# Performance work log

Measured on AMD Instinct MI355X. Metric: run time of the kernel, lower is better.

Reference implementation:

```python
import jax, jax.numpy as jnp
import numpy as np

S, DIM, DE = 8192, 256, 256


def setup_inputs() -> dict:
    key = jax.random.key(0)
    kx, kq, kk, kv = jax.random.split(key, 4)
    x = jax.random.normal(kx, (S, DE), dtype=jnp.float32)
    # tf.random_normal_initializer() default: stddev=0.05
    Wq = jax.random.normal(kq, (DIM, DE), dtype=jnp.float32) * 0.05
    Wk = jax.random.normal(kk, (DIM, DE), dtype=jnp.float32) * 0.05
    Wv = jax.random.normal(kv, (DE, DE), dtype=jnp.float32) * 0.05
    return {"x": x, "Wq": Wq, "Wk": Wk, "Wv": Wv}


def reference(x, Wq, Wk, Wv):
    # x: [S, De]; Wq, Wk: [dim, De]; Wv: [De, De]
    dim = Wq.shape[0]
    Q = Wq @ x.T                                   # [dim, S]
    K = Wk @ x.T                                   # [dim, S]
    score = (Q.T @ K) / jnp.sqrt(jnp.float32(dim))  # [S, S]
    s = score.shape[0]
    # band_part(-1, 0) keeps the lower triangle (causal); zeros elsewhere,
    # then tf.where(score != 0, score, float64.min) -> mask upper triangle
    # with a huge negative (float64.min underflows to -inf in fp32; use fp32 min).
    causal = jnp.tril(jnp.ones((s, s), dtype=bool))
    score = jnp.where(causal, score, jnp.finfo(score.dtype).min)
    attn = jax.nn.softmax(score, axis=1)           # softmax over key axis per row
    V = Wv @ x.T                                   # [De, S]
    deltaE = attn @ V.T                            # [S, De]
    return deltaE
```

## Files before the change

### kernel.cpp

```cpp
#include <hip/hip_runtime.h>
#include <hip/hip_bf16.h>

typedef __attribute__((ext_vector_type(8))) short bf16x8;
typedef __attribute__((ext_vector_type(8))) unsigned short u16x8;
typedef __attribute__((ext_vector_type(4))) float f32x4;

#define SEQ   8192
#define DEM   256
#define CHUNK 512
#define NTASKS 544

#define GLOAD_LDS16(g, l) \
  __builtin_amdgcn_global_load_lds((const __attribute__((address_space(1))) void*)(g), \
                                   (__attribute__((address_space(3))) void*)(l), 16, 0, 0)

static __device__ __forceinline__ unsigned short f2bf(float f) {
  union { float f; unsigned int u; } v; v.f = f;
  return (unsigned short)((v.u + 0x7fffu + ((v.u >> 16) & 1u)) >> 16);
}
static __device__ __forceinline__ float bf2f(unsigned short h) {
  union { unsigned int u; float f; } v; v.u = ((unsigned int)h) << 16;
  return v.f;
}

__global__ __launch_bounds__(256) void proj_kernel(
    const float* __restrict__ x,  const float* __restrict__ Wq,
    const float* __restrict__ Wk, const float* __restrict__ Wv,
    unsigned short* __restrict__ qb, unsigned short* __restrict__ kb,
    unsigned short* __restrict__ vtb)
{
  const int m0 = blockIdx.x * 128;
  const int n0 = blockIdx.y * 128;
  const int which = blockIdx.z;
  const float* __restrict__ W = (which == 0) ? Wq : (which == 1) ? Wk : Wv;

  __shared__ unsigned short As[128 * 64];
  __shared__ unsigned short Bs[128 * 64];

  const int tid  = threadIdx.x;
  const int wave = tid >> 6, lane = tid & 63;
  const int wm = wave >> 1, wn = wave & 1;
  const int lr = lane & 15, lg = lane >> 4;

  f32x4 acc[4][4];
  #pragma unroll
  for (int i = 0; i < 4; i++)
    #pragma unroll
    for (int j = 0; j < 4; j++) acc[i][j] = (f32x4){0.f, 0.f, 0.f, 0.f};

  for (int k0 = 0; k0 < DEM; k0 += 64) {
    __syncthreads();
    #pragma unroll
    for (int p = 0; p < 8; p++) {
      int c   = p * 256 + tid;
      int row = c >> 4;
      int col = (c & 15) << 2;
      float4 fA = *reinterpret_cast<const float4*>(&x[(m0 + row) * DEM + k0 + col]);
      float4 fB = *reinterpret_cast<const float4*>(&W[(n0 + row) * DEM + k0 + col]);
      uint2 hA, hB;
      hA.x = f2bf(fA.x) | ((unsigned)f2bf(fA.y) << 16);
      hA.y = f2bf(fA.z) | ((unsigned)f2bf(fA.w) << 16);
      hB.x = f2bf(fB.x) | ((unsigned)f2bf(fB.y) << 16);
      hB.y = f2bf(fB.z) | ((unsigned)f2bf(fB.w) << 16);
      int byte = (row * 128 + (col << 1)) ^ ((row & 7) << 4);
      *reinterpret_cast<uint2*>(reinterpret_cast<char*>(As) + byte) = hA;
      *reinterpret_cast<uint2*>(reinterpret_cast<char*>(Bs) + byte) = hB;
    }
    __syncthreads();

    #pragma unroll
    for (int ks = 0; ks < 2; ks++) {
      bf16x8 a[4], b[4];
      #pragma unroll
      for (int mt = 0; mt < 4; mt++) {
        int row  = wm * 64 + mt * 16 + lr;
        int byte = (row * 128 + ks * 64 + lg * 16) ^ ((row & 7) << 4);
        a[mt] = *reinterpret_cast<const bf16x8*>(reinterpret_cast<const char*>(As) + byte);
      }
      #pragma unroll
      for (int nt = 0; nt < 4; nt++) {
        int row  = wn * 64 + nt * 16 + lr;
        int byte = (row * 128 + ks * 64 + lg * 16) ^ ((row & 7) << 4);
        b[nt] = *reinterpret_cast<const bf16x8*>(reinterpret_cast<const char*>(Bs) + byte);
      }
      #pragma unroll
      for (int mt = 0; mt < 4; mt++)
        #pragma unroll
        for (int nt = 0; nt < 4; nt++)
          acc[mt][nt] = __builtin_amdgcn_mfma_f32_16x16x32_bf16(a[mt], b[nt], acc[mt][nt], 0, 0, 0);
    }
  }

  const float osc = (which == 0) ? 0.0625f : 1.0f;
  #pragma unroll
  for (int mt = 0; mt < 4; mt++)
    #pragma unroll
    for (int nt = 0; nt < 4; nt++)
      #pragma unroll
      for (int r = 0; r < 4; r++) {
        int row = m0 + wm * 64 + mt * 16 + lg * 4 + r;
        int col = n0 + wn * 64 + nt * 16 + lr;
        unsigned short h = f2bf(acc[mt][nt][r] * osc);
        if (which == 0)      qb[row * DEM + col]  = h;
        else if (which == 1) kb[row * DEM + col]  = h;
        else                 vtb[(size_t)col * SEQ + row] = h;
      }
}

__global__ __launch_bounds__(512, 2) void attn_kernel(
    const unsigned short* __restrict__ qb, const unsigned short* __restrict__ kb,
    const unsigned short* __restrict__ vtb,
    unsigned short* __restrict__ pOb, float* __restrict__ ml)
{
  __shared__ char lds[147456];
  char* Ks = lds;
  char* Vs = lds + 65536;
  char* Ps = lds + 131072;

  const int t = NTASKS - 1 - (int)blockIdx.x;
  int q = 0, s = 0;
  for (;;) { int n = (q >> 2) + 1; if (t < s + n) break; s += n; ++q; }
  const int c = t - s;
  const int kv_lo = c * CHUNK;
  const int kv_hi_blk = min(kv_lo + CHUNK, (q + 1) * 128);

  const int tid = threadIdx.x;
  const int wave = tid >> 6, lane = tid & 63;
  const int lr = lane & 15, lg = lane >> 4;
  const int qrow = q * 128 + wave * 16;
  const int kv_hi_w = min(kv_hi_blk, ((qrow + 16 + 63) >> 6) << 6);
  char* pb = Ps + wave * 2048;

  bf16x8 qf[8];
  {
    const unsigned short* qp = qb + (size_t)(qrow + lr) * DEM + lg * 8;
    #pragma unroll
    for (int ks = 0; ks < 8; ks++) qf[ks] = *reinterpret_cast<const bf16x8*>(qp + ks * 32);
  }

  f32x4 o[16];
  #pragma unroll
  for (int d = 0; d < 16; d++) o[d] = (f32x4){0.f, 0.f, 0.f, 0.f};
  float m_run = -3.0e38f, l_run = 0.f;

  #pragma unroll
  for (int i = 0; i < 4; i++) {
    int sl = i * 8192 + (wave << 10) + (lane << 4);
    int krow = sl >> 9;
    int kin  = (sl & 511) ^ ((krow & 7) << 4);
    GLOAD_LDS16((const char*)kb + (((size_t)(kv_lo + krow)) << 9) + kin,
                Ks + i * 8192 + (wave << 10));
    int vrow = sl >> 7;
    int vin  = (sl & 127) ^ ((vrow & 7) << 4);
    GLOAD_LDS16((const char*)vtb + ((size_t)vrow * SEQ + kv_lo) * 2 + vin,
                Vs + i * 8192 + (wave << 10));
  }
  __syncthreads();

  const int nsteps = (kv_hi_blk - kv_lo) >> 6;
  for (int st = 0; st < nsteps; st++) {
    const int kv0 = kv_lo + (st << 6);
    const int buf = st & 1;
    if (st + 1 < nsteps) {
      #pragma unroll
      for (int i = 0; i < 4; i++) {
        int sl = i * 8192 + (wave << 10) + (lane << 4);
        int krow = sl >> 9;
        int kin  = (sl & 511) ^ ((krow & 7) << 4);
        GLOAD_LDS16((const char*)kb + (((size_t)(kv0 + 64 + krow)) << 9) + kin,
                    Ks + (buf ^ 1) * 32768 + i * 8192 + (wave << 10));
        int vrow = sl >> 7;
        int vin  = (sl & 127) ^ ((vrow & 7) << 4);
        GLOAD_LDS16((const char*)vtb + ((size_t)vrow * SEQ + kv0 + 64) * 2 + vin,
                    Vs + (buf ^ 1) * 32768 + i * 8192 + (wave << 10));
      }
    }

    const bool act = kv0 < kv_hi_w;
    if (act) {
      f32x4 sc[4];
      #pragma unroll
      for (int nt = 0; nt < 4; nt++) sc[nt] = (f32x4){0.f, 0.f, 0.f, 0.f};
      const char* kbase = Ks + buf * 32768;
      __builtin_amdgcn_s_setprio(1);
      #pragma unroll
      for (int ks = 0; ks < 8; ks++)
        #pragma unroll
        for (int nt = 0; nt < 4; nt++) {
          int krow = nt * 16 + lr;
          int byte = krow * 512 + ((ks * 64 + lg * 16) ^ ((krow & 7) << 4));
          bf16x8 kf = *reinterpret_cast<const bf16x8*>(kbase + byte);
          sc[nt] = __builtin_amdgcn_mfma_f32_16x16x32_bf16(kf, qf[ks], sc[nt], 0, 0, 0);
        }
      __builtin_amdgcn_s_setprio(0);

      const int qg = qrow + lr;
      const bool diag = (kv0 + 63 > qrow);
      float sm[16];
      #pragma unroll
      for (int nt = 0; nt < 4; nt++)
        #pragma unroll
        for (int r = 0; r < 4; r++) {
          float v = sc[nt][r];
          if (diag && (kv0 + nt * 16 + lg * 4 + r > qg)) v = -3.0e38f;
          sm[nt * 4 + r] = v;
        }
      float mx = sm[0];
      #pragma unroll
      for (int j = 1; j < 16; j++) mx = fmaxf(mx, sm[j]);
      mx = fmaxf(mx, __shfl_xor(mx, 16));
      mx = fmaxf(mx, __shfl_xor(mx, 32));
      const float mnew = fmaxf(m_run, mx);
      const float cr = __expf(m_run - mnew);
      float e[16], sum = 0.f;
      #pragma unroll
      for (int j = 0; j < 16; j++) { e[j] = __expf(sm[j] - mnew); sum += e[j]; }
      sum += __shfl_xor(sum, 16);
      sum += __shfl_xor(sum, 32);
      m_run = mnew;
      l_run = l_run * cr + sum;

      #pragma unroll
      for (int nt = 0; nt < 4; nt++) {
        uint2 w;
        w.x = (unsigned)f2bf(e[nt * 4 + 0]) | ((unsigned)f2bf(e[nt * 4 + 1]) << 16);
        w.y = (unsigned)f2bf(e[nt * 4 + 2]) | ((unsigned)f2bf(e[nt * 4 + 3]) << 16);
        *reinterpret_cast<uint2*>(pb + (lr * 128 + ((nt * 32 + lg * 8) ^ ((lr & 7) << 4)))) = w;
      }

      float cf[4];
      #pragma unroll
      for (int r = 0; r < 4; r++) cf[r] = __shfl(cr, lg * 4 + r);
      #pragma unroll
      for (int d = 0; d < 16; d++)
        #pragma unroll
        for (int r = 0; r < 4; r++) o[d][r] *= cf[r];

      bf16x8 pf0 = *reinterpret_cast<const bf16x8*>(pb + (lr * 128 + ((lg * 16)      ^ ((lr & 7) << 4))));
      bf16x8 pf1 = *reinterpret_cast<const bf16x8*>(pb + (lr * 128 + ((64 + lg * 16) ^ ((lr & 7) << 4))));
      const char* vbase = Vs + buf * 32768;
      __builtin_amdgcn_s_setprio(1);
      #pragma unroll
      for (int d = 0; d < 16; d++) {
        const int vrow = d * 16 + lr;
        const int vswz = (vrow & 7) << 4;
        bf16x8 v0 = *reinterpret_cast<const bf16x8*>(vbase + vrow * 128 + ((lg * 16)      ^ vswz));
        bf16x8 v1 = *reinterpret_cast<const bf16x8*>(vbase + vrow * 128 + ((64 + lg * 16) ^ vswz));
        o[d] = __builtin_amdgcn_mfma_f32_16x16x32_bf16(pf0, v0, o[d], 0, 0, 0);
        o[d] = __builtin_amdgcn_mfma_f32_16x16x32_bf16(pf1, v1, o[d], 0, 0, 0);
      }
      __builtin_amdgcn_s_setprio(0);
    }
    __syncthreads();
  }

  const size_t obase = (size_t)t * (128 * 256);
  #pragma unroll
  for (int d = 0; d < 16; d++)
    #pragma unroll
    for (int r = 0; r < 4; r++) {
      const int row_l = wave * 16 + lg * 4 + r;
      pOb[obase + (size_t)row_l * 256 + d * 16 + lr] = f2bf(o[d][r]);
    }
  if (lg == 0) {
    const int row_l = wave * 16 + lr;
    ml[(size_t)t * 256 + row_l * 2]     = m_run;
    ml[(size_t)t * 256 + row_l * 2 + 1] = l_run;
  }
}

__global__ __launch_bounds__(256) void merge_kernel(
    const unsigned short* __restrict__ pOb, const float* __restrict__ ml,
    float* __restrict__ out)
{
  const int tid = threadIdx.x;
  const int row = blockIdx.x * 32 + (tid >> 3);
  const int c0  = (tid & 7) * 32;
  const int q = row >> 7;
  const int a = q >> 2, b = q & 3;
  const int n = a + 1;
  const int base = (2 * a + b) * (a + 1);
  const int lrow = row & 127;

  float M = -3.0e38f;
  for (int i = 0; i < n; i++)
    M = fmaxf(M, ml[(size_t)(base + i) * 256 + lrow * 2]);

  float L = 0.f;
  float acc[32];
  #pragma unroll
  for (int j = 0; j < 32; j++) acc[j] = 0.f;

  for (int i = 0; i < n; i++) {
    const float mi = ml[(size_t)(base + i) * 256 + lrow * 2];
    const float li = ml[(size_t)(base + i) * 256 + lrow * 2 + 1];
    const float fi = __expf(mi - M);
    L += li * fi;
    const unsigned short* src = pOb + (size_t)(base + i) * (128 * 256) + (size_t)lrow * 256 + c0;
    #pragma unroll
    for (int v = 0; v < 4; v++) {
      u16x8 u = *reinterpret_cast<const u16x8*>(src + v * 8);
      #pragma unroll
      for (int j = 0; j < 8; j++) acc[v * 8 + j] += bf2f((unsigned short)u[j]) * fi;
    }
  }
  const float inv = 1.f / L;
  #pragma unroll
  for (int v = 0; v < 8; v++) {
    float4 w;
    w.x = acc[v * 4 + 0] * inv; w.y = acc[v * 4 + 1] * inv;
    w.z = acc[v * 4 + 2] * inv; w.w = acc[v * 4 + 3] * inv;
    *reinterpret_cast<float4*>(&out[(size_t)row * 256 + c0 + v * 4]) = w;
  }
}

extern "C" void kernel_launch(void* const* d_in, const int* in_sizes, int n_in,
                              void* d_out, int out_size, void* d_ws, size_t ws_size,
                              hipStream_t stream)
{
  const float* x  = (const float*)d_in[0];
  const float* Wq = (const float*)d_in[1];
  const float* Wk = (const float*)d_in[2];
  const float* Wv = (const float*)d_in[3];

  char* ws = (char*)d_ws;
  unsigned short* qb  = (unsigned short*)ws;
  unsigned short* kb  = (unsigned short*)(ws + (size_t)4  * 1024 * 1024);
  unsigned short* vtb = (unsigned short*)(ws + (size_t)8  * 1024 * 1024);
  float*          ml  = (float*)         (ws + (size_t)12 * 1024 * 1024);
  unsigned short* pOb = (unsigned short*)(ws + (size_t)13 * 1024 * 1024);

  proj_kernel<<<dim3(64, 2, 3), 256, 0, stream>>>(x, Wq, Wk, Wv, qb, kb, vtb);
  attn_kernel<<<dim3(NTASKS), 512, 0, stream>>>(qb, kb, vtb, pOb, ml);
  merge_kernel<<<dim3(SEQ / 32), 256, 0, stream>>>(pOb, ml, (float*)d_out);
}
```

Before: 125.7 us.

## Switch attention to 32x32 MFMA tiles with 256-row query blocks and lazy rescale

Each attention block now covers 256 query rows (32 per wave), which halves the task count. It uses 32x32x16 bf16 MFMA for both the QK^T and PV products, so each K/V tile loaded into LDS is reused across more query rows. The log2(e) factor is folded into the Q scale so the softmax can use exp2 directly. Output rescaling is skipped when the row max grows by no more than a threshold. The merge kernel's indexing is updated to match. The larger per-wave accumulators raise register pressure, and fewer, larger causal tasks may balance less well across CUs.

```diff
diff --git a/kernel.cpp b/kernel.cpp
--- a/kernel.cpp
+++ b/kernel.cpp
@@ -4,11 +4,12 @@
 typedef __attribute__((ext_vector_type(8))) short bf16x8;
 typedef __attribute__((ext_vector_type(8))) unsigned short u16x8;
 typedef __attribute__((ext_vector_type(4))) float f32x4;
+typedef __attribute__((ext_vector_type(16))) float f32x16;
 
 #define SEQ   8192
 #define DEM   256
 #define CHUNK 512
-#define NTASKS 544
+#define NTASKS 272
 
 #define GLOAD_LDS16(g, l) \
   __builtin_amdgcn_global_load_lds((const __attribute__((address_space(1))) void*)(g), \
@@ -91,7 +92,7 @@
     }
   }
 
-  const float osc = (which == 0) ? 0.0625f : 1.0f;
+  const float osc = (which == 0) ? 0.0625f * 1.4426950408889634f : 1.0f;
   #pragma unroll
   for (int mt = 0; mt < 4; mt++)
     #pragma unroll
@@ -119,33 +120,36 @@
 
   const int t = NTASKS - 1 - (int)blockIdx.x;
   int q = 0, s = 0;
-  for (;;) { int n = (q >> 2) + 1; if (t < s + n) break; s += n; ++q; }
+  for (;;) { int n = (q >> 1) + 1; if (t < s + n) break; s += n; ++q; }
   const int c = t - s;
   const int kv_lo = c * CHUNK;
-  const int kv_hi_blk = min(kv_lo + CHUNK, (q + 1) * 128);
+  const int kv_hi_blk = min(kv_lo + CHUNK, (q + 1) * 256);
 
   const int tid = threadIdx.x;
   const int wave = tid >> 6, lane = tid & 63;
-  const int lr = lane & 15, lg = lane >> 4;
-  const int qrow = q * 128 + wave * 16;
-  const int kv_hi_w = min(kv_hi_blk, ((qrow + 16 + 63) >> 6) << 6);
+  const int ql = lane & 31;
+  const int hi = lane >> 5;
+  const int qrow = q * 256 + wave * 32;
+  const int kv_hi_w = min(kv_hi_blk, ((qrow + 32 + 63) >> 6) << 6);
   char* pb = Ps + wave * 2048;
 
-  bf16x8 qf[8];
+  bf16x8 qf[16];
   {
-    const unsigned short* qp = qb + (size_t)(qrow + lr) * DEM + lg * 8;
-    #pragma unroll
-    for (int ks = 0; ks < 8; ks++) qf[ks] = *reinterpret_cast<const bf16x8*>(qp + ks * 32);
-  }
-
-  f32x4 o[16];
-  #pragma unroll
-  for (int d = 0; d < 16; d++) o[d] = (f32x4){0.f, 0.f, 0.f, 0.f};
+    const unsigned short* qp = qb + (size_t)(qrow + ql) * DEM + hi * 8;
+    #pragma unroll
+    for (int i = 0; i < 16; i++) qf[i] = *reinterpret_cast<const bf16x8*>(qp + i * 16);
+  }
+
+  f32x16 o[8];
+  #pragma unroll
+  for (int dt = 0; dt < 8; dt++)
+    #pragma unroll
+    for (int rg = 0; rg < 16; rg++) o[dt][rg] = 0.f;
   float m_run = -3.0e38f, l_run = 0.f;
 
   #pragma unroll
   for (int i = 0; i < 4; i++) {
-    int sl = i * 8192 + (wave << 10) + (lane << 4);
+    int sl = i * 8192 + tid * 16;
     int krow = sl >> 9;
     int kin  = (sl & 511) ^ ((krow & 7) << 4);
     GLOAD_LDS16((const char*)kb + (((size_t)(kv_lo + krow)) << 9) + kin,
@@ -164,7 +168,7 @@
     if (st + 1 < nsteps) {
       #pragma unroll
       for (int i = 0; i < 4; i++) {
-        int sl = i * 8192 + (wave << 10) + (lane << 4);
+        int sl = i * 8192 + tid * 16;
         int krow = sl >> 9;
         int kin  = (sl & 511) ^ ((krow & 7) << 4);
         GLOAD_LDS16((const char*)kb + (((size_t)(kv0 + 64 + krow)) << 9) + kin,
@@ -178,94 +182,114 @@
 
     const bool act = kv0 < kv_hi_w;
     if (act) {
-      f32x4 sc[4];
-      #pragma unroll
-      for (int nt = 0; nt < 4; nt++) sc[nt] = (f32x4){0.f, 0.f, 0.f, 0.f};
+      f32x16 sc0, sc1;
+      #pragma unroll
+      for (int rg = 0; rg < 16; rg++) { sc0[rg] = 0.f; sc1[rg] = 0.f; }
       const char* kbase = Ks + buf * 32768;
+      const int r0 = ql, r1 = 32 + ql;
+      const int rsw = (ql & 7) << 4;
       __builtin_amdgcn_s_setprio(1);
       #pragma unroll
-      for (int ks = 0; ks < 8; ks++)
-        #pragma unroll
-        for (int nt = 0; nt < 4; nt++) {
-          int krow = nt * 16 + lr;
-          int byte = krow * 512 + ((ks * 64 + lg * 16) ^ ((krow & 7) << 4));
-          bf16x8 kf = *reinterpret_cast<const bf16x8*>(kbase + byte);
-          sc[nt] = __builtin_amdgcn_mfma_f32_16x16x32_bf16(kf, qf[ks], sc[nt], 0, 0, 0);
+      for (int i = 0; i < 16; i++) {
+        int off = (i * 32 + hi * 16) ^ rsw;
+        bf16x8 kf0 = *reinterpret_cast<const bf16x8*>(kbase + r0 * 512 + off);
+        bf16x8 kf1 = *reinterpret_cast<const bf16x8*>(kbase + r1 * 512 + off);
+        sc0 = __builtin_amdgcn_mfma_f32_32x32x16_bf16(kf0, qf[i], sc0, 0, 0, 0);
+        sc1 = __builtin_amdgcn_mfma_f32_32x32x16_bf16(kf1, qf[i], sc1, 0, 0, 0);
+      }
+      __builtin_amdgcn_s_setprio(0);
+
+      const int qg = qrow + ql;
+      if (kv0 + 63 > qrow) {
+        #pragma unroll
+        for (int rg = 0; rg < 16; rg++) {
+          int kvp = kv0 + (rg & 3) + 8 * (rg >> 2) + 4 * hi;
+          if (kvp      > qg) sc0[rg] = -3.0e38f;
+          if (kvp + 32 > qg) sc1[rg] = -3.0e38f;
         }
-      __builtin_amdgcn_s_setprio(0);
-
-      const int qg = qrow + lr;
-      const bool diag = (kv0 + 63 > qrow);
-      float sm[16];
-      #pragma unroll
-      for (int nt = 0; nt < 4; nt++)
-        #pragma unroll
-        for (int r = 0; r < 4; r++) {
-          float v = sc[nt][r];
-          if (diag && (kv0 + nt * 16 + lg * 4 + r > qg)) v = -3.0e38f;
-          sm[nt * 4 + r] = v;
+      }
+      float pmax = fmaxf(sc0[0], sc1[0]);
+      #pragma unroll
+      for (int rg = 1; rg < 16; rg++) pmax = fmaxf(pmax, fmaxf(sc0[rg], sc1[rg]));
+      pmax = fmaxf(pmax, __shfl_xor(pmax, 32));
+
+      float mnew;
+      if (__all(pmax <= m_run + 11.0f)) {
+        mnew = m_run;
+      } else {
+        mnew = fmaxf(m_run, pmax);
+        const float cr = __builtin_amdgcn_exp2f(m_run - mnew);
+        #pragma unroll
+        for (int dt = 0; dt < 8; dt++)
+          #pragma unroll
+          for (int rg = 0; rg < 16; rg++) o[dt][rg] *= cr;
+        l_run *= cr;
+        m_run = mnew;
+      }
+
+      float sum = 0.f;
+      uint2 w0[4], w1[4];
+      #pragma unroll
+      for (int tq = 0; tq < 4; tq++) {
+        float e00 = __builtin_amdgcn_exp2f(sc0[tq*4+0] - mnew);
+        float e01 = __builtin_amdgcn_exp2f(sc0[tq*4+1] - mnew);
+        float e02 = __builtin_amdgcn_exp2f(sc0[tq*4+2] - mnew);
+        float e03 = __builtin_amdgcn_exp2f(sc0[tq*4+3] - mnew);
+        float e10 = __builtin_amdgcn_exp2f(sc1[tq*4+0] - mnew);
+        float e11 = __builtin_amdgcn_exp2f(sc1[tq*4+1] - mnew);
+        float e12 = __builtin_amdgcn_exp2f(sc1[tq*4+2] - mnew);
+        float e13 = __builtin_amdgcn_exp2f(sc1[tq*4+3] - mnew);
+        sum += (e00 + e01) + (e02 + e03) + (e10 + e11) + (e12 + e13);
+        w0[tq].x = (unsigned)f2bf(e00) | ((unsigned)f2bf(e01) << 16);
+        w0[tq].y = (unsigned)f2bf(e02) | ((unsigned)f2bf(e03) << 16);
+        w1[tq].x = (unsigned)f2bf(e10) | ((unsigned)f2bf(e11) << 16);
+        w1[tq].y = (unsigned)f2bf(e12) | ((unsigned)f2bf(e13) << 16);
+      }
+      sum += __shfl_xor(sum, 32);
+      l_run += sum;
+
+      const char* vbase = Vs + buf * 32768;
+      const int psw = (ql & 3) << 4;
+      #pragma unroll
+      for (int sub = 0; sub < 2; sub++) {
+        #pragma unroll
+        for (int tq = 0; tq < 4; tq++)
+          *reinterpret_cast<uint2*>(pb + ql * 64 + ((tq * 16 + hi * 8) ^ psw)) =
+              sub ? w1[tq] : w0[tq];
+        bf16x8 pf0 = *reinterpret_cast<const bf16x8*>(pb + ql * 64 + ((hi * 16) ^ psw));
+        bf16x8 pf1 = *reinterpret_cast<const bf16x8*>(pb + ql * 64 + ((32 + hi * 16) ^ psw));
+        __builtin_amdgcn_s_setprio(1);
+        #pragma unroll
+        for (int dt = 0; dt < 8; dt++) {
+          const int vrow = dt * 32 + ql;
+          const char* vp = vbase + vrow * 128;
+          const int vsw = (vrow & 7) << 4;
+          bf16x8 vf0 = *reinterpret_cast<const bf16x8*>(vp + ((sub * 64 + hi * 16) ^ vsw));
+          bf16x8 vf1 = *reinterpret_cast<const bf16x8*>(vp + ((sub * 64 + 32 + hi * 16) ^ vsw));
+          o[dt] = __builtin_amdgcn_mfma_f32_32x32x16_bf16(vf0, pf0, o[dt], 0, 0, 0);
+          o[dt] = __builtin_amdgcn_mfma_f32_32x32x16_bf16(vf1, pf1, o[dt], 0, 0, 0);
         }
-      float mx = sm[0];
-      #pragma unroll
-      for (int j = 1; j < 16; j++) mx = fmaxf(mx, sm[j]);
-      mx = fmaxf(mx, __shfl_xor(mx, 16));
-      mx = fmaxf(mx, __shfl_xor(mx, 32));
-      const float mnew = fmaxf(m_run, mx);
-      const float cr = __expf(m_run - mnew);
-      float e[16], sum = 0.f;
-      #pragma unroll
-      for (int j = 0; j < 16; j++) { e[j] = __expf(sm[j] - mnew); sum += e[j]; }
-      sum += __shfl_xor(sum, 16);
-      sum += __shfl_xor(sum, 32);
-      m_run = mnew;
-      l_run = l_run * cr + sum;
-
-      #pragma unroll
-      for (int nt = 0; nt < 4; nt++) {
-        uint2 w;
-        w.x = (unsigned)f2bf(e[nt * 4 + 0]) | ((unsigned)f2bf(e[nt * 4 + 1]) << 16);
-        w.y = (unsigned)f2bf(e[nt * 4 + 2]) | ((unsigned)f2bf(e[nt * 4 + 3]) << 16);
-        *reinterpret_cast<uint2*>(pb + (lr * 128 + ((nt * 32 + lg * 8) ^ ((lr & 7) << 4)))) = w;
-      }
-
-      float cf[4];
-      #pragma unroll
-      for (int r = 0; r < 4; r++) cf[r] = __shfl(cr, lg * 4 + r);
-      #pragma unroll
-      for (int d = 0; d < 16; d++)
-        #pragma unroll
-        for (int r = 0; r < 4; r++) o[d][r] *= cf[r];
-
-      bf16x8 pf0 = *reinterpret_cast<const bf16x8*>(pb + (lr * 128 + ((lg * 16)      ^ ((lr & 7) << 4))));
-      bf16x8 pf1 = *reinterpret_cast<const bf16x8*>(pb + (lr * 128 + ((64 + lg * 16) ^ ((lr & 7) << 4))));
-      const char* vbase = Vs + buf * 32768;
-      __builtin_amdgcn_s_setprio(1);
-      #pragma unroll
-      for (int d = 0; d < 16; d++) {
-        const int vrow = d * 16 + lr;
-        const int vswz = (vrow & 7) << 4;
-        bf16x8 v0 = *reinterpret_cast<const bf16x8*>(vbase + vrow * 128 + ((lg * 16)      ^ vswz));
-        bf16x8 v1 = *reinterpret_cast<const bf16x8*>(vbase + vrow * 128 + ((64 + lg * 16) ^ vswz));
-        o[d] = __builtin_amdgcn_mfma_f32_16x16x32_bf16(pf0, v0, o[d], 0, 0, 0);
-        o[d] = __builtin_amdgcn_mfma_f32_16x16x32_bf16(pf1, v1, o[d], 0, 0, 0);
-      }
-      __builtin_amdgcn_s_setprio(0);
+        __builtin_amdgcn_s_setprio(0);
+      }
     }
     __syncthreads();
   }
 
-  const size_t obase = (size_t)t * (128 * 256);
-  #pragma unroll
-  for (int d = 0; d < 16; d++)
-    #pragma unroll
-    for (int r = 0; r < 4; r++) {
-      const int row_l = wave * 16 + lg * 4 + r;
-      pOb[obase + (size_t)row_l * 256 + d * 16 + lr] = f2bf(o[d][r]);
-    }
-  if (lg == 0) {
-    const int row_l = wave * 16 + lr;
-    ml[(size_t)t * 256 + row_l * 2]     = m_run;
-    ml[(size_t)t * 256 + row_l * 2 + 1] = l_run;
+  const size_t obase = (size_t)t * (256 * 256);
+  const int row_l = wave * 32 + ql;
+  #pragma unroll
+  for (int dt = 0; dt < 8; dt++)
+    #pragma unroll
+    for (int tq = 0; tq < 4; tq++) {
+      const int d = dt * 32 + tq * 8 + hi * 4;
+      uint2 w;
+      w.x = (unsigned)f2bf(o[dt][tq*4+0]) | ((unsigned)f2bf(o[dt][tq*4+1]) << 16);
+      w.y = (unsigned)f2bf(o[dt][tq*4+2]) | ((unsigned)f2bf(o[dt][tq*4+3]) << 16);
+      *reinterpret_cast<uint2*>(&pOb[obase + (size_t)row_l * 256 + d]) = w;
+    }
+  if (hi == 0) {
+    ml[(size_t)t * 512 + row_l * 2]     = m_run;
+    ml[(size_t)t * 512 + row_l * 2 + 1] = l_run;
   }
 }
 
@@ -276,15 +300,15 @@
   const int tid = threadIdx.x;
   const int row = blockIdx.x * 32 + (tid >> 3);
   const int c0  = (tid & 7) * 32;
-  const int q = row >> 7;
-  const int a = q >> 2, b = q & 3;
+  const int q = row >> 8;
+  const int a = q >> 1, b = q & 1;
   const int n = a + 1;
-  const int base = (2 * a + b) * (a + 1);
-  const int lrow = row & 127;
+  const int base = (a + b) * (a + 1);
+  const int lrow = row & 255;
 
   float M = -3.0e38f;
   for (int i = 0; i < n; i++)
-    M = fmaxf(M, ml[(size_t)(base + i) * 256 + lrow * 2]);
+    M = fmaxf(M, ml[(size_t)(base + i) * 512 + lrow * 2]);
 
   float L = 0.f;
   float acc[32];
@@ -292,11 +316,11 @@
   for (int j = 0; j < 32; j++) acc[j] = 0.f;
 
   for (int i = 0; i < n; i++) {
-    const float mi = ml[(size_t)(base + i) * 256 + lrow * 2];
-    const float li = ml[(size_t)(base + i) * 256 + lrow * 2 + 1];
-    const float fi = __expf(mi - M);
+    const float mi = ml[(size_t)(base + i) * 512 + lrow * 2];
+    const float li = ml[(size_t)(base + i) * 512 + lrow * 2 + 1];
+    const float fi = __builtin_amdgcn_exp2f(mi - M);
     L += li * fi;
-    const unsigned short* src = pOb + (size_t)(base + i) * (128 * 256) + (size_t)lrow * 256 + c0;
+    const unsigned short* src = pOb + (size_t)(base + i) * (256 * 256) + (size_t)lrow * 256 + c0;
     #pragma unroll
     for (int v = 0; v < 4; v++) {
       u16x8 u = *reinterpret_cast<const u16x8*>(src + v * 8);
```

New measurement: 170.6 us. 1.36x slower.
